# Kernel tuning notes

Measured on AMD Instinct MI355X. Metric: run time of the kernel, lower is better.

Reference implementation:

```python
import jax, jax.numpy as jnp
import numpy as np

B, IN_F, OUT_F, K = 8192, 1024, 4096, 2
S = 64  # sqrt(OUT_F)


def setup_inputs() -> dict:
    key = jax.random.key(0)
    k1, k2, k3, k4 = jax.random.split(key, 4)
    x = jax.random.normal(k1, (B, IN_F), dtype=jnp.float32)
    y = jax.random.normal(k2, (B, OUT_F), dtype=jnp.float32)
    weight = jax.random.normal(k3, (OUT_F, IN_F), dtype=jnp.float32) * (1.0 / np.sqrt(IN_F))
    bias = jax.random.normal(k4, (OUT_F,), dtype=jnp.float32) * (1.0 / np.sqrt(IN_F))
    return {"x": x, "y": y, "weight": weight, "bias": bias}


def reference(x, y, weight, bias):
    # fused GEMM + bias + residual add epilogue
    out_lin = jnp.einsum('bk,nk->bn', x, weight) + bias + y  # (B, OUT_F)
    feat = out_lin.reshape(B, S, S)
    # AvgPool2d(kernel=K, stride=K)
    s_out = S // K
    pooled = feat.reshape(B, s_out, K, s_out, K).mean(axis=(2, 4))  # (B, s_out, s_out)
    # divide by global mean of the pooled map
    mean_val = pooled.mean()
    normed = pooled / mean_val
    return normed[:, None, :, :]  # (B, 1, s_out, s_out)
```

## Files before the change

kernel.cpp:

```cpp
#include <hip/hip_runtime.h>
#include <stdint.h>


#define KDIM 1024
#define NP   1024
#define BM 128
#define BN 128
#define BK 64

typedef __bf16 bf16x8 __attribute__((ext_vector_type(8)));
typedef float f32x4 __attribute__((ext_vector_type(4)));
typedef _Float16 f16x4 __attribute__((ext_vector_type(4)));

__device__ __forceinline__ unsigned f2bf(float f) {
  union { float f; unsigned u; } v; v.f = f;
  unsigned r = v.u + 0x7fffu + ((v.u >> 16) & 1u);
  return r >> 16;
}

__device__ __forceinline__ void gload_lds16(const void* g, void* l) {
  __builtin_amdgcn_global_load_lds(
      (const __attribute__((address_space(1))) void*)g,
      (__attribute__((address_space(3))) void*)l, 16, 0, 0);
}

__global__ void k_prep(const float* __restrict__ x, const float* __restrict__ W,
                       const float* __restrict__ bias,
                       unsigned short* __restrict__ xb, unsigned short* __restrict__ wp,
                       float* __restrict__ biasp) {
  int b = blockIdx.x;
  int t = threadIdx.x;
  if (b < 4096) {
    int i = b * 256 + t;
    const float4* x4 = (const float4*)x;
    float4 a = x4[i * 2], c = x4[i * 2 + 1];
    uint4 o;
    o.x = f2bf(a.x) | (f2bf(a.y) << 16);
    o.y = f2bf(a.z) | (f2bf(a.w) << 16);
    o.z = f2bf(c.x) | (f2bf(c.y) << 16);
    o.w = f2bf(c.z) | (f2bf(c.w) << 16);
    ((uint4*)xb)[i] = o;
  } else {
    int o = b - 4096;
    int r0 = ((o >> 5) << 7) + ((o & 31) << 1);
    const float4* W4 = (const float4*)W;
    float4 w0 = W4[(r0) * 256 + t];
    float4 w1 = W4[(r0 + 1) * 256 + t];
    float4 w2 = W4[(r0 + 64) * 256 + t];
    float4 w3 = W4[(r0 + 65) * 256 + t];
    float ax = 0.25f * (w0.x + w1.x + w2.x + w3.x);
    float ay = 0.25f * (w0.y + w1.y + w2.y + w3.y);
    float az = 0.25f * (w0.z + w1.z + w2.z + w3.z);
    float aw = 0.25f * (w0.w + w1.w + w2.w + w3.w);
    uint2 pk;
    pk.x = f2bf(ax) | (f2bf(ay) << 16);
    pk.y = f2bf(az) | (f2bf(aw) << 16);
    ((uint2*)wp)[o * 256 + t] = pk;
    if (t == 0)
      biasp[o] = 0.25f * (bias[r0] + bias[r0 + 1] + bias[r0 + 64] + bias[r0 + 65]);
  }
}

__global__ __launch_bounds__(512) void k_gemm(
    const unsigned short* __restrict__ xb, const unsigned short* __restrict__ wp,
    const float* __restrict__ biasp, const float* __restrict__ y,
    float* __restrict__ out, _Float16* __restrict__ ph,
    float* __restrict__ partials, int use16) {
  __shared__ char smem[65536];

  int bid = blockIdx.x;
  int wg = (bid & 7) * 64 + (bid >> 3);
  int bm0 = (wg >> 3) * BM;
  int bn0 = (wg & 7) * BN;

  int tid = threadIdx.x;
  int lane = tid & 63;
  int wid = tid >> 6;
  int wr = wid >> 1, wc = wid & 1;

  f32x4 acc[2][4];
#pragma unroll
  for (int i = 0; i < 2; i++)
#pragma unroll
    for (int j = 0; j < 4; j++) acc[i][j] = (f32x4)0.0f;

  int srow = tid >> 3;
  int scol = (((lane & 7) ^ (lane >> 3)) << 3);
  const unsigned short* aSrc = xb + (size_t)(bm0 + srow) * KDIM + scol;
  const unsigned short* bSrc = wp + (size_t)(bn0 + srow) * KDIM + scol;
  int ldsOff = wid * 1024;

  int rbase = (lane & 15) * 128;
  int xorv = (lane & 7) << 4;
  int cb0 = (((lane >> 4) * 16)) ^ xorv;
  int cb1 = ((64 + (lane >> 4) * 16)) ^ xorv;

#define STAGE(buf, ks)                                                         \
  {                                                                            \
    int k0 = (ks) * BK;                                                        \
    char* ab = smem + (buf) * 32768 + ldsOff;                                  \
    char* bb = smem + (buf) * 32768 + 16384 + ldsOff;                          \
    _Pragma("unroll")                                                          \
    for (int i = 0; i < 2; ++i)                                                \
      gload_lds16(aSrc + (size_t)i * 64 * KDIM + k0, ab + i * 8192);           \
    _Pragma("unroll")                                                          \
    for (int i = 0; i < 2; ++i)                                                \
      gload_lds16(bSrc + (size_t)i * 64 * KDIM + k0, bb + i * 8192);           \
  }

  STAGE(0, 0);
  for (int ks = 0; ks < 16; ++ks) {
    int cur = ks & 1;
    if (ks < 15) {
      STAGE(cur ^ 1, ks + 1);
      asm volatile("s_waitcnt vmcnt(4)" ::: "memory");
    } else {
      asm volatile("s_waitcnt vmcnt(0)" ::: "memory");
    }
    __builtin_amdgcn_s_barrier();
    asm volatile("" ::: "memory");
    const char* Ab = smem + cur * 32768;
    const char* Bb = Ab + 16384;
#pragma unroll
    for (int kk = 0; kk < 2; ++kk) {
      int cb = kk ? cb1 : cb0;
      bf16x8 af[2], bfr[4];
#pragma unroll
      for (int mi = 0; mi < 2; ++mi)
        af[mi] = *(const bf16x8*)(Ab + (wr * 32 + mi * 16) * 128 + rbase + cb);
#pragma unroll
      for (int ni = 0; ni < 4; ++ni)
        bfr[ni] = *(const bf16x8*)(Bb + (wc * 64 + ni * 16) * 128 + rbase + cb);
#pragma unroll
      for (int mi = 0; mi < 2; ++mi)
#pragma unroll
        for (int ni = 0; ni < 4; ++ni)
          acc[mi][ni] = __builtin_amdgcn_mfma_f32_16x16x32_bf16(af[mi], bfr[ni], acc[mi][ni], 0, 0, 0);
    }
    asm volatile("" ::: "memory");
    __builtin_amdgcn_s_barrier();
  }

  const float2* y2 = (const float2*)y;
  float tsum = 0.f;
  int r_l = (lane >> 4) * 4;
  int c_l = lane & 15;
#pragma unroll
  for (int mi = 0; mi < 2; ++mi) {
#pragma unroll
    for (int ni = 0; ni < 4; ++ni) {
      int col = bn0 + wc * 64 + ni * 16 + c_l;
      float bp = biasp[col];
      int y2base = ((col >> 5) << 6) + (col & 31);
#pragma unroll
      for (int j = 0; j < 4; ++j) {
        int row = bm0 + wr * 32 + mi * 16 + r_l + j;
        float2 u = y2[(size_t)row * 2048 + y2base];
        float2 v = y2[(size_t)row * 2048 + y2base + 32];
        float val = acc[mi][ni][j] + bp + 0.25f * (u.x + u.y + v.x + v.y);
        size_t idx = (size_t)row * NP + col;
        if (use16) ph[idx] = (_Float16)val;
        else out[idx] = val;
        tsum += val;
      }
    }
  }
#pragma unroll
  for (int off = 32; off > 0; off >>= 1) tsum += __shfl_down(tsum, off);
  float* sm = (float*)smem;
  __syncthreads();
  if (lane == 0) sm[wid] = tsum;
  __syncthreads();
  if (tid == 0)
    partials[bid] = ((sm[0] + sm[1]) + (sm[2] + sm[3])) +
                    ((sm[4] + sm[5]) + (sm[6] + sm[7]));
}

__global__ void k_norm(float* __restrict__ out, const _Float16* __restrict__ ph,
                       const float* __restrict__ partials, int use16) {
  __shared__ float s[256];
  int t = threadIdx.x;
  s[t] = partials[t] + partials[t + 256];
  __syncthreads();
#pragma unroll
  for (int off = 128; off > 0; off >>= 1) {
    if (t < off) s[t] += s[t + off];
    __syncthreads();
  }
  float inv = 8388608.0f / s[0];
  int i = blockIdx.x * 256 + t;
  float4* o4 = (float4*)out;
  if (use16) {
    f16x4 hv = ((const f16x4*)ph)[i];
    float4 v;
    v.x = (float)hv[0] * inv;
    v.y = (float)hv[1] * inv;
    v.z = (float)hv[2] * inv;
    v.w = (float)hv[3] * inv;
    o4[i] = v;
  } else {
    float4 v = o4[i];
    v.x *= inv; v.y *= inv; v.z *= inv; v.w *= inv;
    o4[i] = v;
  }
}

extern "C" void kernel_launch(void* const* d_in, const int* in_sizes, int n_in,
                              void* d_out, int out_size, void* d_ws, size_t ws_size,
                              hipStream_t stream) {
  (void)in_sizes; (void)n_in; (void)out_size;
  const float* x = (const float*)d_in[0];
  const float* y = (const float*)d_in[1];
  const float* W = (const float*)d_in[2];
  const float* bias = (const float*)d_in[3];
  float* out = (float*)d_out;

  char* ws = (char*)d_ws;
  unsigned short* xb = (unsigned short*)(ws);
  unsigned short* wp = (unsigned short*)(ws + 16777216);
  float* biasp = (float*)(ws + 16777216 + 2097152);
  float* partials = (float*)(ws + 16777216 + 2097152 + 4096);
  _Float16* ph = (_Float16*)(ws + 20971520);
  int use16 = (ws_size >= (size_t)20971520 + 16777216) ? 1 : 0;

  hipLaunchKernelGGL(k_prep, dim3(5120), dim3(256), 0, stream, x, W, bias, xb, wp, biasp);
  hipLaunchKernelGGL(k_gemm, dim3(512), dim3(512), 0, stream, xb, wp, biasp, y, out, ph, partials, use16);
  hipLaunchKernelGGL(k_norm, dim3(8192), dim3(256), 0, stream, out, ph, partials, use16);
}
```

Before: 62.13 us.

## Overlap residual y loads with GEMM main loop via software-pipelined prefetch

Moves the epilogue's residual-tensor (y) loads into the K loop. Each iteration issues two rows' worth of y loads with inline asm and folds them into the accumulators two iterations later, using a three-deep register ring and adjusted vmcnt waits. The goal is to hide the 128 MB y read latency behind MFMA work instead of stalling in the epilogue. It also adds a launch-bounds occupancy hint of 4. In exchange it raises register pressure, and it relies on hand-tuned waitcnt counts that must match the exact number of outstanding loads.

```diff
diff --git a/kernel.cpp b/kernel.cpp
--- a/kernel.cpp
+++ b/kernel.cpp
@@ -61,7 +61,7 @@
   }
 }
 
-__global__ __launch_bounds__(512) void k_gemm(
+__global__ __launch_bounds__(512, 4) void k_gemm(
     const unsigned short* __restrict__ xb, const unsigned short* __restrict__ wp,
     const float* __restrict__ biasp, const float* __restrict__ y,
     float* __restrict__ out, _Float16* __restrict__ ph,
@@ -94,6 +94,18 @@
   int xorv = (lane & 7) << 4;
   int cb0 = (((lane >> 4) * 16)) ^ xorv;
   int cb1 = ((64 + (lane >> 4) * 16)) ^ xorv;
+
+  const float2* y2 = (const float2*)y;
+  int r_l = (lane >> 4) * 4;
+  int c_l = lane & 15;
+  int yrow0 = bm0 + wr * 32 + r_l;
+  int yb[4];
+#pragma unroll
+  for (int ni = 0; ni < 4; ++ni) {
+    int col = bn0 + wc * 64 + ni * 16 + c_l;
+    yb[ni] = ((col >> 5) << 6) + (col & 31);
+  }
+  float2 yin[3][4];
 
 #define STAGE(buf, ks)                                                         \
   {                                                                            \
@@ -108,59 +120,100 @@
       gload_lds16(bSrc + (size_t)i * 64 * KDIM + k0, bb + i * 8192);           \
   }
 
+#define YLD(p, s, q)                                                           \
+  {                                                                            \
+    const float2* pp = y2 +                                                    \
+        (size_t)(yrow0 + (((q) >> 4) * 16) + ((q) & 3)) * 2048 +               \
+        yb[((q) >> 2) & 3];                                                    \
+    asm volatile("global_load_dwordx2 %0, %1, off"                             \
+                 : "=v"(yin[(p) % 3][s]) : "v"(pp) : "memory");                \
+    asm volatile("global_load_dwordx2 %0, %1, off offset:256"                  \
+                 : "=v"(yin[(p) % 3][(s) + 1]) : "v"(pp) : "memory");          \
+  }
+#define YLOAD(p) { YLD(p, 0, 2 * (p)) YLD(p, 2, 2 * (p) + 1) }
+#define YCONS(p)                                                               \
+  {                                                                            \
+    acc[(2 * (p)) >> 4][((2 * (p)) >> 2) & 3][(2 * (p)) & 3] +=                \
+        0.25f * ((yin[(p) % 3][0].x + yin[(p) % 3][0].y) +                     \
+                 (yin[(p) % 3][1].x + yin[(p) % 3][1].y));                     \
+    acc[(2 * (p) + 1) >> 4][((2 * (p) + 1) >> 2) & 3][(2 * (p) + 1) & 3] +=    \
+        0.25f * ((yin[(p) % 3][2].x + yin[(p) % 3][2].y) +                     \
+                 (yin[(p) % 3][3].x + yin[(p) % 3][3].y));                     \
+  }
+
+#define COMPUTE(cur)                                                           \
+  {                                                                            \
+    const char* Ab = smem + (cur) * 32768;                                     \
+    const char* Bb = Ab + 16384;                                               \
+    _Pragma("unroll")                                                          \
+    for (int kk = 0; kk < 2; ++kk) {                                           \
+      int cb = kk ? cb1 : cb0;                                                 \
+      bf16x8 af[2], bfr[4];                                                    \
+      _Pragma("unroll")                                                        \
+      for (int mi = 0; mi < 2; ++mi)                                           \
+        af[mi] = *(const bf16x8*)(Ab + (wr * 32 + mi * 16) * 128 + rbase + cb);\
+      _Pragma("unroll")                                                        \
+      for (int ni = 0; ni < 4; ++ni)                                           \
+        bfr[ni] = *(const bf16x8*)(Bb + (wc * 64 + ni * 16) * 128 + rbase + cb);\
+      _Pragma("unroll")                                                        \
+      for (int mi = 0; mi < 2; ++mi)                                           \
+        _Pragma("unroll")                                                      \
+        for (int ni = 0; ni < 4; ++ni)                                         \
+          acc[mi][ni] = __builtin_amdgcn_mfma_f32_16x16x32_bf16(               \
+              af[mi], bfr[ni], acc[mi][ni], 0, 0, 0);                          \
+    }                                                                          \
+  }
+
+#define KITER(ks, WAITSTR)                                                     \
+  {                                                                            \
+    if ((ks) < 15) STAGE(((ks) + 1) & 1, (ks) + 1);                            \
+    YLOAD(ks);                                                                 \
+    asm volatile(WAITSTR ::: "memory");                                        \
+    __builtin_amdgcn_s_barrier();                                              \
+    COMPUTE((ks) & 1);                                                         \
+    __builtin_amdgcn_sched_barrier(0);                                         \
+    if ((ks) >= 2) YCONS(((ks) >= 2 ? (ks) - 2 : 0));                          \
+    asm volatile("" ::: "memory");                                             \
+    __builtin_amdgcn_s_barrier();                                              \
+  }
+
   STAGE(0, 0);
-  for (int ks = 0; ks < 16; ++ks) {
-    int cur = ks & 1;
-    if (ks < 15) {
-      STAGE(cur ^ 1, ks + 1);
-      asm volatile("s_waitcnt vmcnt(4)" ::: "memory");
-    } else {
-      asm volatile("s_waitcnt vmcnt(0)" ::: "memory");
-    }
-    __builtin_amdgcn_s_barrier();
-    asm volatile("" ::: "memory");
-    const char* Ab = smem + cur * 32768;
-    const char* Bb = Ab + 16384;
-#pragma unroll
-    for (int kk = 0; kk < 2; ++kk) {
-      int cb = kk ? cb1 : cb0;
-      bf16x8 af[2], bfr[4];
-#pragma unroll
-      for (int mi = 0; mi < 2; ++mi)
-        af[mi] = *(const bf16x8*)(Ab + (wr * 32 + mi * 16) * 128 + rbase + cb);
-#pragma unroll
-      for (int ni = 0; ni < 4; ++ni)
-        bfr[ni] = *(const bf16x8*)(Bb + (wc * 64 + ni * 16) * 128 + rbase + cb);
-#pragma unroll
-      for (int mi = 0; mi < 2; ++mi)
-#pragma unroll
-        for (int ni = 0; ni < 4; ++ni)
-          acc[mi][ni] = __builtin_amdgcn_mfma_f32_16x16x32_bf16(af[mi], bfr[ni], acc[mi][ni], 0, 0, 0);
-    }
-    asm volatile("" ::: "memory");
-    __builtin_amdgcn_s_barrier();
-  }
-
-  const float2* y2 = (const float2*)y;
+  KITER(0,  "s_waitcnt vmcnt(8)")
+  KITER(1,  "s_waitcnt vmcnt(12)")
+  KITER(2,  "s_waitcnt vmcnt(12)")
+  KITER(3,  "s_waitcnt vmcnt(12)")
+  KITER(4,  "s_waitcnt vmcnt(12)")
+  KITER(5,  "s_waitcnt vmcnt(12)")
+  KITER(6,  "s_waitcnt vmcnt(12)")
+  KITER(7,  "s_waitcnt vmcnt(12)")
+  KITER(8,  "s_waitcnt vmcnt(12)")
+  KITER(9,  "s_waitcnt vmcnt(12)")
+  KITER(10, "s_waitcnt vmcnt(12)")
+  KITER(11, "s_waitcnt vmcnt(12)")
+  KITER(12, "s_waitcnt vmcnt(12)")
+  KITER(13, "s_waitcnt vmcnt(12)")
+  KITER(14, "s_waitcnt vmcnt(12)")
+  KITER(15, "s_waitcnt vmcnt(0)")
+  __builtin_amdgcn_sched_barrier(0);
+  YCONS(14);
+  YCONS(15);
+
   float tsum = 0.f;
-  int r_l = (lane >> 4) * 4;
-  int c_l = lane & 15;
+  float bpv[4];
+#pragma unroll
+  for (int ni = 0; ni < 4; ++ni) bpv[ni] = biasp[bn0 + wc * 64 + ni * 16 + c_l];
 #pragma unroll
   for (int mi = 0; mi < 2; ++mi) {
 #pragma unroll
     for (int ni = 0; ni < 4; ++ni) {
       int col = bn0 + wc * 64 + ni * 16 + c_l;
-      float bp = biasp[col];
-      int y2base = ((col >> 5) << 6) + (col & 31);
 #pragma unroll
       for (int j = 0; j < 4; ++j) {
         int row = bm0 + wr * 32 + mi * 16 + r_l + j;
-        float2 u = y2[(size_t)row * 2048 + y2base];
-        float2 v = y2[(size_t)row * 2048 + y2base + 32];
-        float val = acc[mi][ni][j] + bp + 0.25f * (u.x + u.y + v.x + v.y);
-        size_t idx = (size_t)row * NP + col;
-        if (use16) ph[idx] = (_Float16)val;
-        else out[idx] = val;
+        float val = acc[mi][ni][j] + bpv[ni];
+        size_t o = (size_t)row * NP + col;
+        if (use16) ph[o] = (_Float16)val;
+        else out[o] = val;
         tsum += val;
       }
     }
```

Measured after the change: 57.84 us. -6.9%, faster.
